# Optimization experiments

Measured on AMD Instinct MI355X. Metric: run time of the kernel, lower is better.

## Reference

```python
import jax, jax.numpy as jnp
import numpy as np


def _pairwise_dist(x):
    # x: [B, N, D] -> [B, N, N] Euclidean distances (torch.cdist, p=2)
    sq = jnp.sum(x * x, axis=-1)  # [B, N]
    sq_d = sq[:, :, None] + sq[:, None, :] - 2.0 * jnp.einsum('bnd,bmd->bnm', x, x)
    sq_d = jnp.maximum(sq_d, 0.0)
    # safe sqrt (zero diagonal): avoid NaN by masking
    return jnp.where(sq_d > 0.0, jnp.sqrt(jnp.where(sq_d > 0.0, sq_d, 1.0)), 0.0)


def setup_inputs() -> dict:
    key = jax.random.key(0)
    k1, k2, k3 = jax.random.split(key, 3)
    B, N, D = 8, 2048, 3
    preds = jax.random.normal(k1, (B, N, D), dtype=jnp.float32)
    targets = jax.random.normal(k2, (B, N, D), dtype=jnp.float32)
    adj_matrix = jax.random.randint(k3, (B, N, N), 0, 2).astype(jnp.float32)
    return {"preds": preds, "targets": targets, "adj_matrix": adj_matrix}


def reference(preds, targets, adj_matrix):
    dist_preds = _pairwise_dist(preds)      # [B, N, N]
    dist_targets = _pairwise_dist(targets)  # [B, N, N]
    dist = (dist_preds - dist_targets) * adj_matrix
    return jnp.sum(dist * dist) / jnp.sum(adj_matrix)
```

## Files before the change

kernel.cpp:

```cpp
#include <hip/hip_runtime.h>

#define BQ 8
#define NQ 2048
#define ROWS 8
#define TPB 256
#define NBLK (BQ * (NQ / ROWS))
#define JTILE (TPB * 4)
#define NJT (NQ / JTILE)

__global__ __launch_bounds__(TPB, 4) void idla_main(
        const float* __restrict__ preds,
        const float* __restrict__ targets,
        const float* __restrict__ adj,
        float2* __restrict__ partials) {
    __shared__ float red_sq[TPB / 64], red_ad[TPB / 64];

    const int nb_per_batch = NQ / ROWS;
    const int b  = blockIdx.x / nb_per_batch;
    const int i0 = (blockIdx.x % nb_per_batch) * ROWS;
    const int tid = threadIdx.x;

    const float* pb   = preds   + (size_t)b * NQ * 3;
    const float* tb   = targets + (size_t)b * NQ * 3;
    const float* adjb = adj     + (size_t)b * NQ * NQ;

    float acc_sq = 0.0f;
    float acc_ad = 0.0f;

    #pragma unroll
    for (int jt = 0; jt < NJT; ++jt) {
        const int j0 = jt * JTILE + tid * 4;
        const float4* pj = (const float4*)(pb + 3 * j0);
        const float4* tj = (const float4*)(tb + 3 * j0);
        float4 f0 = pj[0], f1 = pj[1], f2 = pj[2];
        float4 g0 = tj[0], g1 = tj[1], g2 = tj[2];
        float jx[4] = {f0.x, f0.w, f1.z, f2.y};
        float jy[4] = {f0.y, f1.x, f1.w, f2.z};
        float jz[4] = {f0.z, f1.y, f2.x, f2.w};
        float ux[4] = {g0.x, g0.w, g1.z, g2.y};
        float uy[4] = {g0.y, g1.x, g1.w, g2.z};
        float uz[4] = {g0.z, g1.y, g2.x, g2.w};

        float4 a4[ROWS];
        #pragma unroll
        for (int r = 0; r < ROWS; ++r)
            a4[r] = *(const float4*)&adjb[(size_t)(i0 + r) * NQ + j0];

        #pragma unroll
        for (int r = 0; r < ROWS; ++r) {
            const int i = i0 + r;
            const float pix = pb[3*i], piy = pb[3*i+1], piz = pb[3*i+2];
            const float tix = tb[3*i], tiy = tb[3*i+1], tiz = tb[3*i+2];
            float av[4] = {a4[r].x, a4[r].y, a4[r].z, a4[r].w};
            #pragma unroll
            for (int jj = 0; jj < 4; ++jj) {
                float dx = pix - jx[jj];
                float dy = piy - jy[jj];
                float dz = piz - jz[jj];
                float sp = fmaf(dx, dx, fmaf(dy, dy, dz * dz));
                float ex = tix - ux[jj];
                float ey = tiy - uy[jj];
                float ez = tiz - uz[jj];
                float st = fmaf(ex, ex, fmaf(ey, ey, ez * ez));
                float rt = __builtin_amdgcn_sqrtf(sp * st);
                float t  = fmaf(-2.0f, rt, sp + st);
                float aa = av[jj] * av[jj];
                acc_sq = fmaf(t, aa, acc_sq);
                acc_ad += av[jj];
            }
        }
    }

    #pragma unroll
    for (int off = 32; off > 0; off >>= 1) {
        acc_sq += __shfl_down(acc_sq, off, 64);
        acc_ad += __shfl_down(acc_ad, off, 64);
    }
    const int wave = tid >> 6;
    if ((tid & 63) == 0) { red_sq[wave] = acc_sq; red_ad[wave] = acc_ad; }
    __syncthreads();
    if (tid == 0) {
        float s_sq = 0.0f, s_ad = 0.0f;
        #pragma unroll
        for (int w = 0; w < TPB / 64; w++) { s_sq += red_sq[w]; s_ad += red_ad[w]; }
        partials[blockIdx.x] = make_float2(s_sq, s_ad);
    }
}

__global__ __launch_bounds__(256) void idla_reduce(
        const float2* __restrict__ partials, float* __restrict__ out) {
    double s = 0.0, a = 0.0;
    for (int i = threadIdx.x; i < NBLK; i += 256) {
        float2 p = partials[i];
        s += (double)p.x;
        a += (double)p.y;
    }
    #pragma unroll
    for (int off = 32; off > 0; off >>= 1) {
        s += __shfl_down(s, off, 64);
        a += __shfl_down(a, off, 64);
    }
    __shared__ double rs[4], ra[4];
    const int wave = threadIdx.x >> 6;
    if ((threadIdx.x & 63) == 0) { rs[wave] = s; ra[wave] = a; }
    __syncthreads();
    if (threadIdx.x == 0) {
        double ts = rs[0] + rs[1] + rs[2] + rs[3];
        double ta = ra[0] + ra[1] + ra[2] + ra[3];
        out[0] = (float)(ts / ta);
    }
}

extern "C" void kernel_launch(void* const* d_in, const int* in_sizes, int n_in,
                              void* d_out, int out_size, void* d_ws, size_t ws_size,
                              hipStream_t stream) {
    const float* preds   = (const float*)d_in[0];
    const float* targets = (const float*)d_in[1];
    const float* adj     = (const float*)d_in[2];
    float2* partials = (float2*)d_ws;
    float*  out      = (float*)d_out;

    hipLaunchKernelGGL(idla_main, dim3(NBLK), dim3(TPB), 0, stream,
                       preds, targets, adj, partials);
    hipLaunchKernelGGL(idla_reduce, dim3(1), dim3(256), 0, stream, partials, out);
}
```

Measured before the change: 194.2 us.

## Retile blocks over j-tiles and 16-row chunks with double-buffered nontemporal adj loads

Each block now covers one 1024-column j tile and 16 rows instead of 8 rows across both j tiles, so the per-column point coordinates are loaded once per block. The adjacency rows are streamed with nontemporal loads into two 4-row register buffers that alternate, letting the next loads be in flight while the current rows are computed. This targets HBM latency hiding for the large adj read, which dominates the kernel. The grid size and partial count stay the same, but register pressure from the two buffers could reduce occupancy.

After: 188.2 us (median of 3 runs). 3.1% less time.

```diff
diff --git a/kernel.cpp b/kernel.cpp
--- a/kernel.cpp
+++ b/kernel.cpp
@@ -2,11 +2,49 @@
 
 #define BQ 8
 #define NQ 2048
-#define ROWS 8
 #define TPB 256
-#define NBLK (BQ * (NQ / ROWS))
 #define JTILE (TPB * 4)
 #define NJT (NQ / JTILE)
+#define ICHUNK 16
+#define NIC (NQ / ICHUNK)
+#define NBLK (BQ * NJT * NIC)
+
+typedef float f32x4 __attribute__((ext_vector_type(4)));
+
+#define LOAD4(buf, rbase)                                                     \
+    do {                                                                      \
+        _Pragma("unroll")                                                     \
+        for (int r = 0; r < 4; ++r)                                           \
+            buf[r] = __builtin_nontemporal_load(                              \
+                (const f32x4*)(arow + (size_t)((rbase) + r) * NQ));           \
+    } while (0)
+
+#define COMP4(buf, rbase)                                                     \
+    do {                                                                      \
+        _Pragma("unroll")                                                     \
+        for (int r = 0; r < 4; ++r) {                                         \
+            const int i = (rbase) + r;          \
+            const float pix = pb[3*i], piy = pb[3*i+1], piz = pb[3*i+2];      \
+            const float tix = tb[3*i], tiy = tb[3*i+1], tiz = tb[3*i+2];      \
+            _Pragma("unroll")                                                 \
+            for (int jj = 0; jj < 4; ++jj) {                                  \
+                float dx = pix - jx[jj];                                      \
+                float dy = piy - jy[jj];                                      \
+                float dz = piz - jz[jj];                                      \
+                float sp = fmaf(dx, dx, fmaf(dy, dy, dz * dz));               \
+                float ex = tix - ux[jj];                                      \
+                float ey = tiy - uy[jj];                                      \
+                float ez = tiz - uz[jj];                                      \
+                float st = fmaf(ex, ex, fmaf(ey, ey, ez * ez));               \
+                float rt = __builtin_amdgcn_sqrtf(sp * st);                   \
+                float t  = fmaf(-2.0f, rt, sp + st);                          \
+                float av = buf[r][jj];                                        \
+                float aa = av * av;                                           \
+                acc_sq = fmaf(t, aa, acc_sq);                                 \
+                acc_ad += av;                                                 \
+            }                                                                 \
+        }                                                                     \
+    } while (0)
 
 __global__ __launch_bounds__(TPB, 4) void idla_main(
         const float* __restrict__ preds,
@@ -15,61 +53,42 @@
         float2* __restrict__ partials) {
     __shared__ float red_sq[TPB / 64], red_ad[TPB / 64];
 
-    const int nb_per_batch = NQ / ROWS;
-    const int b  = blockIdx.x / nb_per_batch;
-    const int i0 = (blockIdx.x % nb_per_batch) * ROWS;
+    const int blk = blockIdx.x;
+    const int b   = blk / (NJT * NIC);
+    const int rem = blk % (NJT * NIC);
+    const int jt  = rem / NIC;
+    const int ic  = rem % NIC;
+    const int i0  = ic * ICHUNK;
     const int tid = threadIdx.x;
+    const int j0  = jt * JTILE + tid * 4;
 
     const float* pb   = preds   + (size_t)b * NQ * 3;
     const float* tb   = targets + (size_t)b * NQ * 3;
-    const float* adjb = adj     + (size_t)b * NQ * NQ;
+    const float* arow = adj + (size_t)b * NQ * NQ + j0;
+
+    const float4* pj = (const float4*)(pb + 3 * j0);
+    const float4* tj = (const float4*)(tb + 3 * j0);
+    float4 f0 = pj[0], f1 = pj[1], f2 = pj[2];
+    float4 g0 = tj[0], g1 = tj[1], g2 = tj[2];
+    float jx[4] = {f0.x, f0.w, f1.z, f2.y};
+    float jy[4] = {f0.y, f1.x, f1.w, f2.z};
+    float jz[4] = {f0.z, f1.y, f2.x, f2.w};
+    float ux[4] = {g0.x, g0.w, g1.z, g2.y};
+    float uy[4] = {g0.y, g1.x, g1.w, g2.z};
+    float uz[4] = {g0.z, g1.y, g2.x, g2.w};
 
     float acc_sq = 0.0f;
     float acc_ad = 0.0f;
 
-    #pragma unroll
-    for (int jt = 0; jt < NJT; ++jt) {
-        const int j0 = jt * JTILE + tid * 4;
-        const float4* pj = (const float4*)(pb + 3 * j0);
-        const float4* tj = (const float4*)(tb + 3 * j0);
-        float4 f0 = pj[0], f1 = pj[1], f2 = pj[2];
-        float4 g0 = tj[0], g1 = tj[1], g2 = tj[2];
-        float jx[4] = {f0.x, f0.w, f1.z, f2.y};
-        float jy[4] = {f0.y, f1.x, f1.w, f2.z};
-        float jz[4] = {f0.z, f1.y, f2.x, f2.w};
-        float ux[4] = {g0.x, g0.w, g1.z, g2.y};
-        float uy[4] = {g0.y, g1.x, g1.w, g2.z};
-        float uz[4] = {g0.z, g1.y, g2.x, g2.w};
-
-        float4 a4[ROWS];
-        #pragma unroll
-        for (int r = 0; r < ROWS; ++r)
-            a4[r] = *(const float4*)&adjb[(size_t)(i0 + r) * NQ + j0];
-
-        #pragma unroll
-        for (int r = 0; r < ROWS; ++r) {
-            const int i = i0 + r;
-            const float pix = pb[3*i], piy = pb[3*i+1], piz = pb[3*i+2];
-            const float tix = tb[3*i], tiy = tb[3*i+1], tiz = tb[3*i+2];
-            float av[4] = {a4[r].x, a4[r].y, a4[r].z, a4[r].w};
-            #pragma unroll
-            for (int jj = 0; jj < 4; ++jj) {
-                float dx = pix - jx[jj];
-                float dy = piy - jy[jj];
-                float dz = piz - jz[jj];
-                float sp = fmaf(dx, dx, fmaf(dy, dy, dz * dz));
-                float ex = tix - ux[jj];
-                float ey = tiy - uy[jj];
-                float ez = tiz - uz[jj];
-                float st = fmaf(ex, ex, fmaf(ey, ey, ez * ez));
-                float rt = __builtin_amdgcn_sqrtf(sp * st);
-                float t  = fmaf(-2.0f, rt, sp + st);
-                float aa = av[jj] * av[jj];
-                acc_sq = fmaf(t, aa, acc_sq);
-                acc_ad += av[jj];
-            }
-        }
-    }
+    f32x4 bufA[4], bufB[4];
+    LOAD4(bufA, i0);
+    LOAD4(bufB, i0 + 4);
+    COMP4(bufA, i0);
+    LOAD4(bufA, i0 + 8);
+    COMP4(bufB, i0 + 4);
+    LOAD4(bufB, i0 + 12);
+    COMP4(bufA, i0 + 8);
+    COMP4(bufB, i0 + 12);
 
     #pragma unroll
     for (int off = 32; off > 0; off >>= 1) {
```
